# Kernel tuning notes

Measured on AMD Instinct MI355X. Metric: run time of the kernel, lower is better.

## Reference

```python
import jax, jax.numpy as jnp
import numpy as np

B, S, D = 16, 4096, 64
SCALE = float(np.sqrt(D))  # sqrt(hidden_size)


def setup_inputs() -> dict:
    key = jax.random.key(0)
    kq, kk, kv = jax.random.split(key, 3)
    return {
        "query": jax.random.normal(kq, (B, S, D), dtype=jnp.float32),
        "key": jax.random.normal(kk, (B, S, D), dtype=jnp.float32),
        "value": jax.random.normal(kv, (B, S, D), dtype=jnp.float32),
    }


def reference(query, key, value):
    # energy: [B, S, S]
    energy = jnp.einsum("bqd,bkd->bqk", query, key) / SCALE
    attention = jax.nn.softmax(energy, axis=2)
    return jnp.einsum("bqk,bkd->bqd", attention, value)
```

## Files before the change

kernel.cpp:

```cpp
#include <hip/hip_runtime.h>


#define NBATCH 16
#define SEQ    4096
#define DIM    64
#define BQ     256
#define BK     64
#define NKT    (SEQ / BK)
#define KHALF  (NKT / 2)
#define KSTR   72
#define PSTR   72
#define OELEMS (NBATCH * SEQ * DIM)
#define NROWS  (NBATCH * SEQ)

#define QSCALE 0.180336879f

typedef _Float16 half2_t __attribute__((ext_vector_type(2)));
typedef _Float16 half4_t __attribute__((ext_vector_type(4)));
typedef _Float16 half8_t __attribute__((ext_vector_type(8)));
typedef float    floatx4 __attribute__((ext_vector_type(4)));

__device__ inline float fast_exp2(float x) {
#if __has_builtin(__builtin_amdgcn_exp2f)
  return __builtin_amdgcn_exp2f(x);
#else
  return exp2f(x);
#endif
}
__device__ inline float fast_rcp(float x) {
#if __has_builtin(__builtin_amdgcn_rcpf)
  return __builtin_amdgcn_rcpf(x);
#else
  return 1.0f / x;
#endif
}

__global__ __launch_bounds__(256, 2)
void attn_f16_flash(const float* __restrict__ Qg, const float* __restrict__ Kg,
                    const float* __restrict__ Vg, float* __restrict__ O0g,
                    float* __restrict__ O1g, float* __restrict__ lsg)
{
  __shared__ __align__(16) _Float16 sK[BK * KSTR];
  __shared__ __align__(16) _Float16 sV[DIM * KSTR];
  __shared__ __align__(16) _Float16 sP[4 * 64 * PSTR];

  const int tid  = threadIdx.x;
  const int wave = tid >> 6;
  const int lane = tid & 63;
  const int l16  = lane & 15;
  const int quad = lane >> 4;

  const int dp = tid & 31;
  const int kb = tid >> 5;

  const int bid  = blockIdx.x;
  const int half = bid & 1;
  const int qb   = bid >> 1;
  const int b    = qb >> 4;
  const int qt   = qb & 15;
  const int q0   = qt * BQ + wave * 64;
  const int kt0  = half * KHALF;

  const float* Qb = Qg + ((size_t)b * SEQ + q0) * DIM;
  const float* Kb = Kg + (size_t)b * SEQ * DIM;
  const float* Vb = Vg + (size_t)b * SEQ * DIM;
  float*       Ob = (half ? O1g : O0g) + ((size_t)b * SEQ + q0) * DIM;
  float*       Ls = lsg + half * NROWS + b * SEQ + q0;

  half8_t qf[4][2];
  #pragma unroll
  for (int s = 0; s < 4; ++s)
    #pragma unroll
    for (int c = 0; c < 2; ++c) {
      const float4 f0 = *(const float4*)(Qb + (s * 16 + l16) * DIM + c * 32 + quad * 8);
      const float4 f1 = *(const float4*)(Qb + (s * 16 + l16) * DIM + c * 32 + quad * 8 + 4);
      half8_t h;
      h[0] = (_Float16)(f0.x * QSCALE); h[1] = (_Float16)(f0.y * QSCALE);
      h[2] = (_Float16)(f0.z * QSCALE); h[3] = (_Float16)(f0.w * QSCALE);
      h[4] = (_Float16)(f1.x * QSCALE); h[5] = (_Float16)(f1.y * QSCALE);
      h[6] = (_Float16)(f1.z * QSCALE); h[7] = (_Float16)(f1.w * QSCALE);
      qf[s][c] = h;
    }

  floatx4 oacc[4][4];
  float   lsum[4][4];
  #pragma unroll
  for (int s = 0; s < 4; ++s) {
    #pragma unroll
    for (int n = 0; n < 4; ++n) oacc[s][n] = (floatx4){0.f, 0.f, 0.f, 0.f};
    #pragma unroll
    for (int r = 0; r < 4; ++r) lsum[s][r] = 0.f;
  }

  _Float16* myP = &sP[wave * 64 * PSTR];

  float2 kbuf[8], vbuf[8];

  #define LOAD_TILE(KT)                                                        \
    {                                                                          \
      const float* Kt_ = Kb + (size_t)(KT) * BK * DIM;                         \
      const float* Vt_ = Vb + (size_t)(KT) * BK * DIM;                         \
      _Pragma("unroll")                                                        \
      for (int i = 0; i < 8; ++i) {                                            \
        const int key = kb + i * 8;                                            \
        kbuf[i] = *(const float2*)(Kt_ + key * DIM + dp * 2);                  \
        vbuf[i] = *(const float2*)(Vt_ + key * DIM + dp * 2);                  \
      }                                                                        \
    }

  #define WRITE_TILE()                                                         \
    {                                                                          \
      _Pragma("unroll")                                                        \
      for (int i = 0; i < 8; ++i) {                                            \
        const int key = kb + i * 8;                                            \
        half2_t h;                                                             \
        h[0] = (_Float16)kbuf[i].x; h[1] = (_Float16)kbuf[i].y;                \
        *(half2_t*)&sK[key * KSTR + dp * 2] = h;                               \
      }                                                                        \
      _Pragma("unroll")                                                        \
      for (int ii = 0; ii < 4; ++ii) {                                         \
        const int i  = (ii & 1) + (ii >> 1) * 4;                  \
        const int k1 = kb + i * 8;                                             \
        const int colb = (k1 & 15) * 4 + (k1 >> 4);      \
        const float2 a = vbuf[i];                                              \
        const float2 bb = vbuf[i + 2];                                         \
        half2_t h0; h0[0] = (_Float16)a.x; h0[1] = (_Float16)bb.x;             \
        half2_t h1; h1[0] = (_Float16)a.y; h1[1] = (_Float16)bb.y;             \
        *(half2_t*)&sV[(dp * 2) * KSTR + colb]     = h0;                       \
        *(half2_t*)&sV[(dp * 2 + 1) * KSTR + colb] = h1;                       \
      }                                                                        \
    }

  #define COMPUTE_TILE()                                                       \
    {                                                                          \
      floatx4 sc[4][4];                                                        \
      _Pragma("unroll")                                                        \
      for (int s = 0; s < 4; ++s)                                              \
        _Pragma("unroll")                                                      \
        for (int n = 0; n < 4; ++n) sc[s][n] = (floatx4){0.f, 0.f, 0.f, 0.f};  \
      _Pragma("unroll")                                                        \
      for (int n = 0; n < 4; ++n)                                              \
        _Pragma("unroll")                                                      \
        for (int c = 0; c < 2; ++c) {                                          \
          half8_t bf = *(const half8_t*)&sK[(n * 16 + l16) * KSTR + c * 32 + quad * 8];\
          _Pragma("unroll")                                                    \
          for (int s = 0; s < 4; ++s)                                          \
            sc[s][n] = __builtin_amdgcn_mfma_f32_16x16x32_f16(qf[s][c], bf,    \
                                                              sc[s][n], 0, 0, 0);\
        }                                                                      \
      _Pragma("unroll")                                                        \
      for (int s = 0; s < 4; ++s)                                              \
        _Pragma("unroll")                                                      \
        for (int r = 0; r < 4; ++r) {                                          \
          half4_t ph;                                                          \
          _Pragma("unroll")                                                    \
          for (int n = 0; n < 4; ++n) {                                        \
            float p = fast_exp2(sc[s][n][r]);                                  \
            lsum[s][r] += p;                                                   \
            ph[n] = (_Float16)p;                                               \
          }                                                                    \
          *(half4_t*)&myP[(s * 16 + quad * 4 + r) * PSTR + l16 * 4] = ph;      \
        }                                                                      \
      _Pragma("unroll")                                                        \
      for (int c = 0; c < 2; ++c) {                                            \
        half8_t pf[4];                                                         \
        _Pragma("unroll")                                                      \
        for (int s = 0; s < 4; ++s)                                            \
          pf[s] = *(const half8_t*)&myP[(s * 16 + l16) * PSTR + c * 32 + quad * 8];\
        _Pragma("unroll")                                                      \
        for (int n = 0; n < 4; ++n) {                                          \
          half8_t vf = *(const half8_t*)&sV[(n * 16 + l16) * KSTR + c * 32 + quad * 8];\
          _Pragma("unroll")                                                    \
          for (int s = 0; s < 4; ++s)                                          \
            oacc[s][n] = __builtin_amdgcn_mfma_f32_16x16x32_f16(pf[s], vf,     \
                                                                oacc[s][n], 0, 0, 0);\
        }                                                                      \
      }                                                                        \
    }

  LOAD_TILE(kt0);
  WRITE_TILE();
  __syncthreads();

  #pragma unroll 1
  for (int kt = kt0; kt < kt0 + KHALF - 1; ++kt) {
    LOAD_TILE(kt + 1);
    COMPUTE_TILE();
    __syncthreads();
    WRITE_TILE();
    __syncthreads();
  }
  COMPUTE_TILE();

  #pragma unroll
  for (int s = 0; s < 4; ++s) {
    float rsum[4];
    #pragma unroll
    for (int r = 0; r < 4; ++r) {
      float v = lsum[s][r];
      v += __shfl_xor(v, 1);
      v += __shfl_xor(v, 2);
      v += __shfl_xor(v, 4);
      v += __shfl_xor(v, 8);
      rsum[r] = v;
    }
    if (l16 == 0) {
      #pragma unroll
      for (int r = 0; r < 4; ++r)
        Ls[s * 16 + quad * 4 + r] = rsum[r];
    }
    #pragma unroll
    for (int n = 0; n < 4; ++n)
      #pragma unroll
      for (int r = 0; r < 4; ++r)
        Ob[(s * 16 + quad * 4 + r) * DIM + n * 16 + l16] = oacc[s][n][r];
  }
  #undef LOAD_TILE
  #undef WRITE_TILE
  #undef COMPUTE_TILE
}

__global__ __launch_bounds__(256)
void attn_combine(float* __restrict__ O, const float* __restrict__ O1,
                  const float* __restrict__ lsg)
{
  const int i = blockIdx.x * 256 + threadIdx.x;
  const float* l0 = lsg;
  const float* l1 = lsg + NROWS;
  const int row = i >> 4;
  const float inv = fast_rcp(l0[row] + l1[row]);
  const float4 a  = ((const float4*)O)[i];
  const float4 bb = ((const float4*)O1)[i];
  float4 r;
  r.x = (a.x + bb.x) * inv;
  r.y = (a.y + bb.y) * inv;
  r.z = (a.z + bb.z) * inv;
  r.w = (a.w + bb.w) * inv;
  ((float4*)O)[i] = r;
}

extern "C" void kernel_launch(void* const* d_in, const int* in_sizes, int n_in,
                              void* d_out, int out_size, void* d_ws, size_t ws_size,
                              hipStream_t stream) {
  const float* Q = (const float*)d_in[0];
  const float* K = (const float*)d_in[1];
  const float* V = (const float*)d_in[2];
  float* O  = (float*)d_out;
  float* O1 = (float*)d_ws;
  float* Ls = (float*)d_ws + OELEMS;
  (void)in_sizes; (void)n_in; (void)out_size; (void)ws_size;

  attn_f16_flash<<<dim3(2 * NBATCH * (SEQ / BQ)), dim3(256), 0, stream>>>(Q, K, V, O, O1, Ls);
  attn_combine<<<dim3(OELEMS / 4 / 256), dim3(256), 0, stream>>>(O, O1, Ls);
}
```

Baseline: 182.1 us.

## Double-buffer V tile, swizzle LDS layout, and widen global loads to float4

Splits the per-tile compute into QK/exp and PV phases and double-buffers the V shared-memory tile, so the next tile's K/V writes to LDS can overlap with the PV MFMAs instead of waiting behind a barrier. Replaces the padded LDS layout with an XOR swizzle to avoid bank conflicts without padding. Global loads become float4 per thread with 16-byte half4 LDS stores. The extra V buffer raises LDS use, which could limit occupancy, and the V transpose write pattern changes.

Measured after the change: 324.1 us. 1.78x slower.

```diff
diff --git a/kernel.cpp b/kernel.cpp
--- a/kernel.cpp
+++ b/kernel.cpp
@@ -8,14 +8,12 @@
 #define BK     64
 #define NKT    (SEQ / BK)
 #define KHALF  (NKT / 2)
-#define KSTR   72
 #define PSTR   72
 #define OELEMS (NBATCH * SEQ * DIM)
 #define NROWS  (NBATCH * SEQ)
 
 #define QSCALE 0.180336879f
 
-typedef _Float16 half2_t __attribute__((ext_vector_type(2)));
 typedef _Float16 half4_t __attribute__((ext_vector_type(4)));
 typedef _Float16 half8_t __attribute__((ext_vector_type(8)));
 typedef float    floatx4 __attribute__((ext_vector_type(4)));
@@ -35,13 +33,17 @@
 #endif
 }
 
+__device__ inline int swz(int row, int col) {
+  return row * 64 + ((((col >> 3) ^ ((row >> 1) & 7)) << 3) | (col & 7));
+}
+
 __global__ __launch_bounds__(256, 2)
 void attn_f16_flash(const float* __restrict__ Qg, const float* __restrict__ Kg,
                     const float* __restrict__ Vg, float* __restrict__ O0g,
                     float* __restrict__ O1g, float* __restrict__ lsg)
 {
-  __shared__ __align__(16) _Float16 sK[BK * KSTR];
-  __shared__ __align__(16) _Float16 sV[DIM * KSTR];
+  __shared__ __align__(16) _Float16 sK[64 * 64];
+  __shared__ __align__(16) _Float16 sV[2][64 * 64];
   __shared__ __align__(16) _Float16 sP[4 * 64 * PSTR];
 
   const int tid  = threadIdx.x;
@@ -49,9 +51,10 @@
   const int lane = tid & 63;
   const int l16  = lane & 15;
   const int quad = lane >> 4;
-
-  const int dp = tid & 31;
-  const int kb = tid >> 5;
+  const int hK   = (l16 >> 1) & 7;
+
+  const int t16 = tid & 15;
+  const int kg  = tid >> 4;
 
   const int bid  = blockIdx.x;
   const int half = bid & 1;
@@ -72,13 +75,13 @@
   for (int s = 0; s < 4; ++s)
     #pragma unroll
     for (int c = 0; c < 2; ++c) {
-      const float4 f0 = *(const float4*)(Qb + (s * 16 + l16) * DIM + c * 32 + quad * 8);
-      const float4 f1 = *(const float4*)(Qb + (s * 16 + l16) * DIM + c * 32 + quad * 8 + 4);
+      const floatx4 f0 = *(const floatx4*)(Qb + (s * 16 + l16) * DIM + c * 32 + quad * 8);
+      const floatx4 f1 = *(const floatx4*)(Qb + (s * 16 + l16) * DIM + c * 32 + quad * 8 + 4);
       half8_t h;
-      h[0] = (_Float16)(f0.x * QSCALE); h[1] = (_Float16)(f0.y * QSCALE);
-      h[2] = (_Float16)(f0.z * QSCALE); h[3] = (_Float16)(f0.w * QSCALE);
-      h[4] = (_Float16)(f1.x * QSCALE); h[5] = (_Float16)(f1.y * QSCALE);
-      h[6] = (_Float16)(f1.z * QSCALE); h[7] = (_Float16)(f1.w * QSCALE);
+      #pragma unroll
+      for (int j = 0; j < 4; ++j) h[j] = (_Float16)(f0[j] * QSCALE);
+      #pragma unroll
+      for (int j = 0; j < 4; ++j) h[4 + j] = (_Float16)(f1[j] * QSCALE);
       qf[s][c] = h;
     }
 
@@ -94,45 +97,42 @@
 
   _Float16* myP = &sP[wave * 64 * PSTR];
 
-  float2 kbuf[8], vbuf[8];
+  floatx4 kbuf[4], vbuf[4];
 
   #define LOAD_TILE(KT)                                                        \
-    {                                                                          \
+    do {                                                                       \
       const float* Kt_ = Kb + (size_t)(KT) * BK * DIM;                         \
       const float* Vt_ = Vb + (size_t)(KT) * BK * DIM;                         \
       _Pragma("unroll")                                                        \
-      for (int i = 0; i < 8; ++i) {                                            \
-        const int key = kb + i * 8;                                            \
-        kbuf[i] = *(const float2*)(Kt_ + key * DIM + dp * 2);                  \
-        vbuf[i] = *(const float2*)(Vt_ + key * DIM + dp * 2);                  \
-      }                                                                        \
-    }
-
-  #define WRITE_TILE()                                                         \
-    {                                                                          \
-      _Pragma("unroll")                                                        \
-      for (int i = 0; i < 8; ++i) {                                            \
-        const int key = kb + i * 8;                                            \
-        half2_t h;                                                             \
-        h[0] = (_Float16)kbuf[i].x; h[1] = (_Float16)kbuf[i].y;                \
-        *(half2_t*)&sK[key * KSTR + dp * 2] = h;                               \
-      }                                                                        \
-      _Pragma("unroll")                                                        \
-      for (int ii = 0; ii < 4; ++ii) {                                         \
-        const int i  = (ii & 1) + (ii >> 1) * 4;                  \
-        const int k1 = kb + i * 8;                                             \
-        const int colb = (k1 & 15) * 4 + (k1 >> 4);      \
-        const float2 a = vbuf[i];                                              \
-        const float2 bb = vbuf[i + 2];                                         \
-        half2_t h0; h0[0] = (_Float16)a.x; h0[1] = (_Float16)bb.x;             \
-        half2_t h1; h1[0] = (_Float16)a.y; h1[1] = (_Float16)bb.y;             \
-        *(half2_t*)&sV[(dp * 2) * KSTR + colb]     = h0;                       \
-        *(half2_t*)&sV[(dp * 2 + 1) * KSTR + colb] = h1;                       \
-      }                                                                        \
-    }
-
-  #define COMPUTE_TILE()                                                       \
-    {                                                                          \
+      for (int i = 0; i < 4; ++i) {                                            \
+        const int key = kg + 16 * i;                                           \
+        kbuf[i] = *(const floatx4*)(Kt_ + key * DIM + t16 * 4);                \
+        vbuf[i] = *(const floatx4*)(Vt_ + key * DIM + t16 * 4);                \
+      }                                                                        \
+    } while (0)
+
+  #define WRITE_TILE(VBUF)                                                     \
+    do {                                                                       \
+      _Pragma("unroll")                                                        \
+      for (int i = 0; i < 4; ++i) {             \
+        const int key = kg + 16 * i;                                           \
+        half4_t h;                                                             \
+        _Pragma("unroll")                                                      \
+        for (int j = 0; j < 4; ++j) h[j] = (_Float16)kbuf[i][j];               \
+        *(half4_t*)&sK[swz(key, t16 * 4)] = h;                                 \
+      }                                                                        \
+      _Pragma("unroll")                                                        \
+      for (int e = 0; e < 4; ++e) {             \
+        const int dim = t16 * 4 + e;                                           \
+        half4_t h;                                                             \
+        _Pragma("unroll")                                                      \
+        for (int i = 0; i < 4; ++i) h[i] = (_Float16)vbuf[i][e];               \
+        *(half4_t*)&(VBUF)[swz(dim, kg * 4)] = h;                              \
+      }                                                                        \
+    } while (0)
+
+  #define QK_EXP()                                                             \
+    do {                                                                       \
       floatx4 sc[4][4];                                                        \
       _Pragma("unroll")                                                        \
       for (int s = 0; s < 4; ++s)                                              \
@@ -142,7 +142,8 @@
       for (int n = 0; n < 4; ++n)                                              \
         _Pragma("unroll")                                                      \
         for (int c = 0; c < 2; ++c) {                                          \
-          half8_t bf = *(const half8_t*)&sK[(n * 16 + l16) * KSTR + c * 32 + quad * 8];\
+          half8_t bf = *(const half8_t*)&sK[(n * 16 + l16) * 64 +              \
+                                            (((c * 4 + quad) ^ hK) << 3)];     \
           _Pragma("unroll")                                                    \
           for (int s = 0; s < 4; ++s)                                          \
             sc[s][n] = __builtin_amdgcn_mfma_f32_16x16x32_f16(qf[s][c], bf,    \
@@ -161,6 +162,10 @@
           }                                                                    \
           *(half4_t*)&myP[(s * 16 + quad * 4 + r) * PSTR + l16 * 4] = ph;      \
         }                                                                      \
+    } while (0)
+
+  #define PV(VBUF)                                                             \
+    do {                                                                       \
       _Pragma("unroll")                                                        \
       for (int c = 0; c < 2; ++c) {                                            \
         half8_t pf[4];                                                         \
@@ -169,28 +174,42 @@
           pf[s] = *(const half8_t*)&myP[(s * 16 + l16) * PSTR + c * 32 + quad * 8];\
         _Pragma("unroll")                                                      \
         for (int n = 0; n < 4; ++n) {                                          \
-          half8_t vf = *(const half8_t*)&sV[(n * 16 + l16) * KSTR + c * 32 + quad * 8];\
+          half8_t vf = *(const half8_t*)&(VBUF)[(n * 16 + l16) * 64 +          \
+                                                (((c * 4 + quad) ^ hK) << 3)]; \
           _Pragma("unroll")                                                    \
           for (int s = 0; s < 4; ++s)                                          \
             oacc[s][n] = __builtin_amdgcn_mfma_f32_16x16x32_f16(pf[s], vf,     \
                                                                 oacc[s][n], 0, 0, 0);\
         }                                                                      \
       }                                                                        \
-    }
+    } while (0)
 
   LOAD_TILE(kt0);
-  WRITE_TILE();
+  WRITE_TILE(sV[0]);
   __syncthreads();
+  int vb = 0;
 
   #pragma unroll 1
   for (int kt = kt0; kt < kt0 + KHALF - 1; ++kt) {
     LOAD_TILE(kt + 1);
-    COMPUTE_TILE();
+    QK_EXP();
     __syncthreads();
-    WRITE_TILE();
+    if (vb == 0) {
+      WRITE_TILE(sV[1]);
+      PV(sV[0]);
+    } else {
+      WRITE_TILE(sV[0]);
+      PV(sV[1]);
+    }
     __syncthreads();
-  }
-  COMPUTE_TILE();
+    vb ^= 1;
+  }
+  QK_EXP();
+  if (vb == 0) {
+    PV(sV[0]);
+  } else {
+    PV(sV[1]);
+  }
 
   #pragma unroll
   for (int s = 0; s < 4; ++s) {
@@ -217,7 +236,8 @@
   }
   #undef LOAD_TILE
   #undef WRITE_TILE
-  #undef COMPUTE_TILE
+  #undef QK_EXP
+  #undef PV
 }
 
 __global__ __launch_bounds__(256)
```
